# Performance work log

Hardware: AMD Instinct MI355X
Metric: run time of the kernel (lower is better)

Reference implementation:

```python
import jax, jax.numpy as jnp
import numpy as np

K = 8            # kernel volume = down_ratio^3 = 2^3
N_IN = 40000     # coarse (input) active voxels
N_OUT = 150000   # fine (output/skip) active voxels
C_IN = 128
C_EMB = 128
C_SKIP = 128
EPS = 1e-5


def setup_inputs() -> dict:
    key = jax.random.key(0)
    ks = jax.random.split(key, 8)
    x_feat = jax.random.normal(ks[0], (N_IN, C_IN), dtype=jnp.float32)
    skip_feat = jax.random.normal(ks[1], (N_OUT, C_SKIP), dtype=jnp.float32)
    pair_in = jax.random.randint(ks[2], (K, N_OUT), 0, N_IN, dtype=jnp.int32)
    pair_out = jax.random.randint(ks[3], (K, N_OUT), 0, N_OUT, dtype=jnp.int32)
    W_up = jax.random.normal(ks[4], (K, C_IN, C_EMB), dtype=jnp.float32) * 0.02
    W1 = jax.random.normal(ks[5], (C_SKIP + C_EMB, C_EMB), dtype=jnp.float32) * 0.05
    W2 = jax.random.normal(ks[6], (C_EMB, C_EMB), dtype=jnp.float32) * 0.05
    return {
        "x_feat": x_feat, "skip_feat": skip_feat,
        "pair_in": pair_in, "pair_out": pair_out,
        "W_up": W_up,
        "g0": jnp.ones((C_EMB,), jnp.float32), "b0": jnp.zeros((C_EMB,), jnp.float32),
        "W1": W1, "b1": jnp.zeros((C_EMB,), jnp.float32),
        "g1": jnp.ones((C_EMB,), jnp.float32), "be1": jnp.zeros((C_EMB,), jnp.float32),
        "W2": W2, "b2": jnp.zeros((C_EMB,), jnp.float32),
        "g2": jnp.ones((C_EMB,), jnp.float32), "be2": jnp.zeros((C_EMB,), jnp.float32),
    }


def _bn(x, gamma, beta):
    # BatchNorm1d over the point axis (training-mode batch stats, biased var)
    m = jnp.mean(x, axis=0)
    v = jnp.mean(jnp.square(x - m), axis=0)
    return (x - m) * jax.lax.rsqrt(v + EPS) * gamma + beta


def reference(x_feat, skip_feat, pair_in, pair_out, W_up,
              g0, b0, W1, b1, g1, be1, W2, b2, g2, be2):
    n_out = skip_feat.shape[0]
    # SparseInverseConv3d: gather coarse features, per-offset GEMM, scatter-add
    out = jnp.zeros((n_out, W_up.shape[2]), dtype=x_feat.dtype)
    for k in range(K):  # fixed small kernel volume, structurally distinct weights
        contrib = x_feat[pair_in[k]] @ W_up[k]          # [P, C_emb]
        out = out.at[pair_out[k]].add(contrib)
    up = jax.nn.relu(_bn(out, g0, b0))                  # [N_out, C_emb]

    # fuse: concat([up, skip]) -> Linear/BN/ReLU x2, residual with up
    h = jnp.concatenate([up, skip_feat], axis=1)        # [N_out, C_emb+C_skip]
    h = jax.nn.relu(_bn(h @ W1 + b1, g1, be1))
    h = jax.nn.relu(_bn(h @ W2 + b2, g2, be2))
    return h + up
```

## Files before the change

### kernel.cpp

```cpp
#include <hip/hip_runtime.h>

#define KVOL 8
#define NIN 40000
#define NOUT 150000
#define C 128
#define EPSV 1e-5f
#define NPAIR (KVOL * NOUT)
#define GM ((NOUT + 63) / 64)
#define GM2 ((NOUT + 127) / 128)
#define GUP (NIN / 64)
#define BROWS 128
#define NBUCK ((NOUT + BROWS - 1) / BROWS)
#define NSTR 8
#define SCAP 256
#define BCAP (NSTR * SCAP)
#define GBUCK ((NPAIR + 4095) / 4096)
#define GUPB (GBUCK + GUP)

typedef __attribute__((ext_vector_type(8))) __bf16 bf16x8;
typedef __attribute__((ext_vector_type(4))) float f32x4;
typedef __attribute__((ext_vector_type(8))) unsigned short us8;

__device__ __forceinline__ unsigned short fbf(float f) {
    unsigned u = __float_as_uint(f);
    u += 0x7fffu + ((u >> 16) & 1u);
    return (unsigned short)(u >> 16);
}
__device__ __forceinline__ float bff(unsigned short s) {
    return __uint_as_float(((unsigned)s) << 16);
}

__global__ __launch_bounds__(256) void k_prep_w(
    const float* __restrict__ Wup, const float* __restrict__ W1, const float* __restrict__ W2,
    unsigned short* __restrict__ WT)
{
    int i = blockIdx.x * 256 + threadIdx.x;
    if (i < 11 * 16384) {
        int b = i >> 14, r = i & 16383;
        int k = r >> 7, n = r & 127;
        const float* src = (b < 8) ? (Wup + (size_t)b * 16384)
                         : (b < 10) ? (W1 + (size_t)(b - 8) * 16384) : W2;
        WT[(size_t)b * 16384 + n * 128 + k] = fbf(src[k * 128 + n]);
    }
}

__global__ __launch_bounds__(256) void k_upb(
    const float* __restrict__ x, const unsigned short* __restrict__ WT,
    unsigned short* __restrict__ Y,
    const int* __restrict__ pout, const int* __restrict__ pin,
    int* __restrict__ bcnt, unsigned int* __restrict__ bbuf)
{
    __shared__ __align__(16) unsigned short Alds[64][136];
    __shared__ __align__(16) unsigned short Wlds[128][136];
    const int t = threadIdx.x;

    if (blockIdx.x < GBUCK) {
        int* cnt = (int*)&Alds[0][0];
        int* bas = cnt + NBUCK;
        int* run = bas + NBUCK;
        const int bid = blockIdx.x;
        const int str = bid & (NSTR - 1);
        const int i0 = bid * 4096;
        for (int b = t; b < NBUCK; b += 256) { cnt[b] = 0; run[b] = 0; }
        __syncthreads();
        for (int j = t; j < 4096; j += 256) {
            int i = i0 + j;
            if (i < NPAIR) atomicAdd(&cnt[pout[i] >> 7], 1);
        }
        __syncthreads();
        for (int b = t; b < NBUCK; b += 256) {
            int c = cnt[b];
            bas[b] = c ? atomicAdd(&bcnt[str * NBUCK + b], c) : 0;
        }
        __syncthreads();
        for (int j = t; j < 4096; j += 256) {
            int i = i0 + j;
            if (i < NPAIR) {
                int o = pout[i];
                int k = i / NOUT;
                unsigned e = (unsigned)(k * NIN + pin[i]);
                int b = o >> 7;
                int dst = bas[b] + atomicAdd(&run[b], 1);
                if (dst < SCAP)
                    bbuf[((size_t)str * NBUCK + b) * SCAP + dst] = ((unsigned)(o & 127) << 24) | e;
            }
        }
        return;
    }

    const int wave = t >> 6, lane = t & 63;
    const int l15 = lane & 15, lhi = lane >> 4;
    const int R = (blockIdx.x - GBUCK) * 64;
    const float4* A4 = (const float4*)x;
    #pragma unroll
    for (int j = 0; j < 8; ++j) {
        int idx = t + j * 256;
        int row = idx >> 5, c4 = idx & 31;
        int grow = R + row;
        float4 v = make_float4(0.f, 0.f, 0.f, 0.f);
        if (grow < NIN) v = A4[(size_t)grow * 32 + c4];
        ushort4 o;
        o.x = fbf(v.x); o.y = fbf(v.y); o.z = fbf(v.z); o.w = fbf(v.w);
        *(ushort4*)&Alds[row][c4 * 4] = o;
    }
    __syncthreads();
    bf16x8 af[4];
    #pragma unroll
    for (int kk = 0; kk < 4; ++kk)
        af[kk] = *(const bf16x8*)&Alds[wave * 16 + l15][kk * 32 + lhi * 8];
    for (int k = 0; k < KVOL; ++k) {
        __syncthreads();
        const us8* Wsrc = (const us8*)(WT + (size_t)k * C * C);
        #pragma unroll
        for (int j = 0; j < 8; ++j) {
            int slot = t + j * 256;
            int n = slot >> 4, koff = (slot & 15) * 8;
            *(us8*)&Wlds[n][koff] = Wsrc[slot];
        }
        __syncthreads();
        f32x4 acc[8];
        #pragma unroll
        for (int n = 0; n < 8; ++n) acc[n] = (f32x4){0.f, 0.f, 0.f, 0.f};
        #pragma unroll
        for (int n = 0; n < 8; ++n) {
            #pragma unroll
            for (int kk = 0; kk < 4; ++kk) {
                bf16x8 bfr = *(const bf16x8*)&Wlds[n * 16 + l15][kk * 32 + lhi * 8];
                acc[n] = __builtin_amdgcn_mfma_f32_16x16x32_bf16(af[kk], bfr, acc[n], 0, 0, 0);
            }
        }
        unsigned short* Yk = Y + (size_t)k * NIN * C;
        #pragma unroll
        for (int n = 0; n < 8; ++n) {
            const int col = n * 16 + l15;
            #pragma unroll
            for (int r = 0; r < 4; ++r) {
                int row = R + wave * 16 + lhi * 4 + r;
                if (row < NIN) Yk[(size_t)row * C + col] = fbf(acc[n][r]);
            }
        }
    }
}

template<int PHASES, bool BNIN, bool STATS>
__global__ __launch_bounds__(512) void k_mfma(
    const void* __restrict__ A0v, const void* __restrict__ A1v,
    const unsigned short* __restrict__ WT,
    const float* __restrict__ bias,
    unsigned short* __restrict__ outp, int M,
    const float* __restrict__ bn_stats, const float* __restrict__ bn_g, const float* __restrict__ bn_b,
    float* __restrict__ parts)
{
    __shared__ __align__(16) unsigned short Alds[128][136];
    __shared__ __align__(16) unsigned short Wlds[128][136];
    __shared__ float sscale[C], sshift[C];
    const int t = threadIdx.x;
    const int wave = t >> 6, lane = t & 63;
    const int l15 = lane & 15, lhi = lane >> 4;
    const int R = blockIdx.x * 128;

    if (BNIN) {
        if (t < C) {
            float m = bn_stats[t] * (1.0f / NOUT);
            float var = bn_stats[C + t] * (1.0f / NOUT) - m * m;
            float sc = bn_g[t] * rsqrtf(var + EPSV);
            sscale[t] = sc;
            sshift[t] = fmaf(-m, sc, bn_b[t]);
        }
        __syncthreads();
    }

    f32x4 acc[8];
    #pragma unroll
    for (int n = 0; n < 8; ++n) acc[n] = (f32x4){0.f, 0.f, 0.f, 0.f};

    {
        const us8* Wsrc = (const us8*)WT;
        #pragma unroll
        for (int j = 0; j < 4; ++j) {
            int slot = t + j * 512;
            *(us8*)&Wlds[slot >> 4][(slot & 15) * 8] = Wsrc[slot];
        }
        const us8* A8 = (const us8*)A0v;
        #pragma unroll
        for (int j = 0; j < 4; ++j) {
            int slot = t + j * 512;
            int row = slot >> 4, s15 = slot & 15, koff = s15 * 8;
            int grow = R + row;
            us8 v = (us8){0, 0, 0, 0, 0, 0, 0, 0};
            if (grow < M) v = A8[(size_t)grow * 16 + s15];
            if (BNIN) {
                us8 w;
                #pragma unroll
                for (int i = 0; i < 8; ++i) {
                    float f = fmaxf(fmaf(bff(v[i]), sscale[koff + i], sshift[koff + i]), 0.f);
                    w[i] = fbf(f);
                }
                v = w;
            }
            *(us8*)&Alds[row][koff] = v;
        }
    }
    __syncthreads();

    if constexpr (PHASES == 2) {
        us8 wreg[4];
        float4 areg[8];
        {
            const us8* Wsrc1 = (const us8*)(WT + C * C);
            #pragma unroll
            for (int j = 0; j < 4; ++j) wreg[j] = Wsrc1[t + j * 512];
            const float4* A41 = (const float4*)A1v;
            #pragma unroll
            for (int j = 0; j < 8; ++j) {
                int slot = t + j * 512;
                int row = slot >> 5, c4 = slot & 31;
                int grow = R + row;
                float4 v = make_float4(0.f, 0.f, 0.f, 0.f);
                if (grow < M) v = A41[(size_t)grow * 32 + c4];
                areg[j] = v;
            }
        }
        {
            bf16x8 af[4];
            #pragma unroll
            for (int kk = 0; kk < 4; ++kk)
                af[kk] = *(const bf16x8*)&Alds[wave * 16 + l15][kk * 32 + lhi * 8];
            #pragma unroll
            for (int n = 0; n < 8; ++n) {
                #pragma unroll
                for (int kk = 0; kk < 4; ++kk) {
                    bf16x8 bfr = *(const bf16x8*)&Wlds[n * 16 + l15][kk * 32 + lhi * 8];
                    acc[n] = __builtin_amdgcn_mfma_f32_16x16x32_bf16(af[kk], bfr, acc[n], 0, 0, 0);
                }
            }
        }
        __syncthreads();
        #pragma unroll
        for (int j = 0; j < 4; ++j) {
            int slot = t + j * 512;
            *(us8*)&Wlds[slot >> 4][(slot & 15) * 8] = wreg[j];
        }
        #pragma unroll
        for (int j = 0; j < 8; ++j) {
            int slot = t + j * 512;
            int row = slot >> 5, c4 = slot & 31;
            float4 v = areg[j];
            ushort4 o;
            o.x = fbf(v.x); o.y = fbf(v.y); o.z = fbf(v.z); o.w = fbf(v.w);
            *(ushort4*)&Alds[row][c4 * 4] = o;
        }
        __syncthreads();
    }
    {
        bf16x8 af[4];
        #pragma unroll
        for (int kk = 0; kk < 4; ++kk)
            af[kk] = *(const bf16x8*)&Alds[wave * 16 + l15][kk * 32 + lhi * 8];
        #pragma unroll
        for (int n = 0; n < 8; ++n) {
            #pragma unroll
            for (int kk = 0; kk < 4; ++kk) {
                bf16x8 bfr = *(const bf16x8*)&Wlds[n * 16 + l15][kk * 32 + lhi * 8];
                acc[n] = __builtin_amdgcn_mfma_f32_16x16x32_bf16(af[kk], bfr, acc[n], 0, 0, 0);
            }
        }
    }
    __syncthreads();

    float* sbS = (float*)&Alds[0][0];
    float* sbQ = sbS + 1024;
    #pragma unroll
    for (int n = 0; n < 8; ++n) {
        const int col = n * 16 + l15;
        float bv = bias[col];
        float s = 0.f, q = 0.f;
        #pragma unroll
        for (int r = 0; r < 4; ++r) {
            int row = R + wave * 16 + lhi * 4 + r;
            if (row < M) {
                float v = acc[n][r] + bv;
                outp[(size_t)row * C + col] = fbf(v);
                if (STATS) { s += v; q = fmaf(v, v, q); }
            }
        }
        if (STATS) {
            s += __shfl_xor(s, 16); s += __shfl_xor(s, 32);
            q += __shfl_xor(q, 16); q += __shfl_xor(q, 32);
            if (lane < 16) {
                sbS[wave * 128 + col] = s;
                sbQ[wave * 128 + col] = q;
            }
        }
    }
    if (STATS) {
        __syncthreads();
        if (t < 128) {
            float S = 0.f;
            #pragma unroll
            for (int w = 0; w < 8; ++w) S += sbS[w * 128 + t];
            parts[(size_t)blockIdx.x * 256 + t] = S;
        } else if (t < 256) {
            int cc = t - 128;
            float Q = 0.f;
            #pragma unroll
            for (int w = 0; w < 8; ++w) Q += sbQ[w * 128 + cc];
            parts[(size_t)blockIdx.x * 256 + t] = Q;
        }
    }
}

__global__ __launch_bounds__(256) void k_reduce(const float* __restrict__ parts, int nb,
                                                float* __restrict__ stats)
{
    const int t = threadIdx.x;
    float s0 = 0.f, s1 = 0.f, s2 = 0.f, s3 = 0.f;
    for (int b = blockIdx.x * 4; b < nb; b += gridDim.x * 4) {
        if (b < nb)     s0 += parts[(size_t)b * 256 + t];
        if (b + 1 < nb) s1 += parts[(size_t)(b + 1) * 256 + t];
        if (b + 2 < nb) s2 += parts[(size_t)(b + 2) * 256 + t];
        if (b + 3 < nb) s3 += parts[(size_t)(b + 3) * 256 + t];
    }
    atomicAdd(&stats[t], (s0 + s1) + (s2 + s3));
}

__global__ __launch_bounds__(256) void k_sortgather(
    const int* __restrict__ bcnt, const unsigned int* __restrict__ bbuf,
    const us8* __restrict__ Y8, us8* __restrict__ up8, float* __restrict__ parts)
{
    __shared__ unsigned int pr[BCAP];
    __shared__ unsigned int srt[BCAP];
    __shared__ int cnt[BROWS], sd[BROWS], ofs2[BROWS];
    const int t = threadIdx.x;
    const int b = blockIdx.x;
    int segbase = 0;
    #pragma unroll
    for (int s = 0; s < NSTR; ++s) {
        int ns = min(bcnt[s * NBUCK + b], SCAP);
        const unsigned int* g = bbuf + ((size_t)s * NBUCK + b) * SCAP;
        for (int j = t; j < ns; j += 256) pr[segbase + j] = g[j];
        segbase += ns;
    }
    const int n = segbase;
    if (t < BROWS) cnt[t] = 0;
    __syncthreads();
    for (int j = t; j < n; j += 256) atomicAdd(&cnt[pr[j] >> 24], 1);
    __syncthreads();
    if (t < BROWS) sd[t] = cnt[t];
    __syncthreads();
    for (int off = 1; off < BROWS; off <<= 1) {
        int a = (t < BROWS) ? sd[t] : 0;
        int bb = (t < BROWS && t >= off) ? sd[t - off] : 0;
        __syncthreads();
        if (t < BROWS) sd[t] = a + bb;
        __syncthreads();
    }
    if (t < BROWS) ofs2[t] = sd[t] - cnt[t];
    __syncthreads();
    for (int j = t; j < n; j += 256) {
        unsigned p = pr[j];
        int pos = atomicAdd(&ofs2[p >> 24], 1);
        srt[pos] = p & 0xFFFFFFu;
    }
    __syncthreads();
    const int wave = t >> 6, lane = t & 63;
    const int rl = t >> 4, c8 = t & 15;
    float s8[8], q8[8];
    #pragma unroll
    for (int i = 0; i < 8; ++i) { s8[i] = 0.f; q8[i] = 0.f; }
    #pragma unroll
    for (int it = 0; it < 8; ++it) {
        int r = it * 16 + rl;
        int o = b * BROWS + r;
        if (o < NOUT) {
            int j1 = sd[r], j0 = j1 - cnt[r];
            float a[8];
            #pragma unroll
            for (int i = 0; i < 8; ++i) a[i] = 0.f;
            int j = j0;
            for (; j + 1 < j1; j += 2) {
                unsigned e0 = srt[j], e1 = srt[j + 1];
                us8 u0 = Y8[(size_t)e0 * 16 + c8];
                us8 u1 = Y8[(size_t)e1 * 16 + c8];
                #pragma unroll
                for (int i = 0; i < 8; ++i) a[i] += bff(u0[i]) + bff(u1[i]);
            }
            if (j < j1) {
                unsigned e0 = srt[j];
                us8 u0 = Y8[(size_t)e0 * 16 + c8];
                #pragma unroll
                for (int i = 0; i < 8; ++i) a[i] += bff(u0[i]);
            }
            us8 o8;
            #pragma unroll
            for (int i = 0; i < 8; ++i) {
                o8[i] = fbf(a[i]);
                s8[i] += a[i];
                q8[i] = fmaf(a[i], a[i], q8[i]);
            }
            up8[(size_t)o * 16 + c8] = o8;
        }
    }
    #pragma unroll
    for (int i = 0; i < 8; ++i) {
        s8[i] += __shfl_xor(s8[i], 16); s8[i] += __shfl_xor(s8[i], 32);
        q8[i] += __shfl_xor(q8[i], 16); q8[i] += __shfl_xor(q8[i], 32);
    }
    float* sS = (float*)pr;
    float* sQ = sS + 512;
    if (lane < 16) {
        #pragma unroll
        for (int i = 0; i < 8; ++i) {
            sS[(wave * 16 + c8) * 8 + i] = s8[i];
            sQ[(wave * 16 + c8) * 8 + i] = q8[i];
        }
    }
    __syncthreads();
    if (t < 128) {
        const int cc = t >> 3, ii = t & 7;
        float S = 0.f, Q = 0.f;
        #pragma unroll
        for (int w = 0; w < 4; ++w) {
            S += sS[(w * 16 + cc) * 8 + ii];
            Q += sQ[(w * 16 + cc) * 8 + ii];
        }
        parts[(size_t)b * 256 + t] = S;
        parts[(size_t)b * 256 + 128 + t] = Q;
    }
}

__global__ __launch_bounds__(256) void k_final(
    const us8* __restrict__ h2, const us8* __restrict__ upr, float* __restrict__ out,
    const float* __restrict__ stats2, const float* __restrict__ g2, const float* __restrict__ be2,
    const float* __restrict__ stats0, const float* __restrict__ g0, const float* __restrict__ b0)
{
    __shared__ float sc2[C], sh2[C], sc0[C], sh0[C];
    const int t = threadIdx.x;
    if (t < C) {
        float m2 = stats2[t] * (1.0f / NOUT);
        float v2 = stats2[C + t] * (1.0f / NOUT) - m2 * m2;
        float c2 = g2[t] * rsqrtf(v2 + EPSV);
        sc2[t] = c2; sh2[t] = fmaf(-m2, c2, be2[t]);
        float m0 = stats0[t] * (1.0f / NOUT);
        float v0 = stats0[C + t] * (1.0f / NOUT) - m0 * m0;
        float c0 = g0[t] * rsqrtf(v0 + EPSV);
        sc0[t] = c0; sh0[t] = fmaf(-m0, c0, b0[t]);
    }
    __syncthreads();
    const int idx0 = blockIdx.x * 256 + t;
    const int c8 = idx0 & 15;
    float l2s[8], l2h[8], l0s[8], l0h[8];
    #pragma unroll
    for (int i = 0; i < 8; ++i) {
        l2s[i] = sc2[c8 * 8 + i]; l2h[i] = sh2[c8 * 8 + i];
        l0s[i] = sc0[c8 * 8 + i]; l0h[i] = sh0[c8 * 8 + i];
    }
    const int total = NOUT * 16;
    for (int idx = idx0; idx < total; idx += gridDim.x * 256) {
        us8 h = h2[idx];
        us8 u = upr[idx];
        float o[8];
        #pragma unroll
        for (int i = 0; i < 8; ++i) {
            o[i] = fmaxf(fmaf(bff(h[i]), l2s[i], l2h[i]), 0.f)
                 + fmaxf(fmaf(bff(u[i]), l0s[i], l0h[i]), 0.f);
        }
        float4* dst = (float4*)&out[(size_t)idx * 8];
        dst[0] = make_float4(o[0], o[1], o[2], o[3]);
        dst[1] = make_float4(o[4], o[5], o[6], o[7]);
    }
}

extern "C" void kernel_launch(void* const* d_in, const int* in_sizes, int n_in,
                              void* d_out, int out_size, void* d_ws, size_t ws_size,
                              hipStream_t stream)
{
    const float* x    = (const float*)d_in[0];
    const float* skip = (const float*)d_in[1];
    const int*   pin  = (const int*)d_in[2];
    const int*   pout = (const int*)d_in[3];
    const float* Wup  = (const float*)d_in[4];
    const float* g0   = (const float*)d_in[5];
    const float* b0   = (const float*)d_in[6];
    const float* W1   = (const float*)d_in[7];
    const float* b1   = (const float*)d_in[8];
    const float* g1   = (const float*)d_in[9];
    const float* be1  = (const float*)d_in[10];
    const float* W2   = (const float*)d_in[11];
    const float* b2   = (const float*)d_in[12];
    const float* g2   = (const float*)d_in[13];
    const float* be2  = (const float*)d_in[14];
    float* outp = (float*)d_out;

    char* base = (char*)d_ws;
    unsigned short* Y      = (unsigned short*)base;
    unsigned short* h1     = (unsigned short*)base;
    unsigned short* h2     = (unsigned short*)(base + 40960000);
    unsigned short* up_raw = (unsigned short*)(base + 81920000);
    char* p = base + 81920000 + 38400000;
    unsigned short* WT = (unsigned short*)p; p += (size_t)11 * 16384 * 2;
    unsigned int* bbuf = (unsigned int*)p;  p += (size_t)NSTR * NBUCK * SCAP * 4;
    int* bcnt      = (int*)p; p += (size_t)NSTR * NBUCK * 4;
    float* parts0  = (float*)p; p += (size_t)NBUCK * 256 * 4;
    float* parts1  = (float*)p; p += (size_t)GM * 256 * 4;
    float* parts2  = (float*)p; p += (size_t)GM * 256 * 4;
    float* stats   = (float*)p; p += 3 * 256 * 4;

    hipMemsetAsync(bcnt, 0, (size_t)NSTR * NBUCK * 4, stream);
    hipMemsetAsync(stats, 0, 3 * 256 * 4, stream);

    k_prep_w<<<(11 * 16384 + 255) / 256, 256, 0, stream>>>(Wup, W1, W2, WT);

    k_upb<<<GUPB, 256, 0, stream>>>(x, WT, Y, pout, pin, bcnt, bbuf);

    k_sortgather<<<NBUCK, 256, 0, stream>>>(bcnt, bbuf, (const us8*)Y, (us8*)up_raw, parts0);
    k_reduce<<<16, 256, 0, stream>>>(parts0, NBUCK, stats);

    k_mfma<2, true, true><<<GM2, 512, 0, stream>>>(
        up_raw, skip, WT + (size_t)8 * 16384, b1, h1, NOUT, stats, g0, b0, parts1);
    k_reduce<<<16, 256, 0, stream>>>(parts1, GM2, stats + 256);

    k_mfma<1, true, true><<<GM2, 512, 0, stream>>>(
        h1, nullptr, WT + (size_t)10 * 16384, b2, h2, NOUT, stats + 256, g1, be1, parts2);
    k_reduce<<<16, 256, 0, stream>>>(parts2, GM2, stats + 512);

    k_final<<<1024, 256, 0, stream>>>((const us8*)h2, (const us8*)up_raw, outp,
        stats + 512, g2, be2, stats, g0, b0);
}
```

Before: 301.5 us.

## Split bucketing from up-GEMM, halve bucket size, stage GEMM outputs through LDS

Splits the fused bucket/up-projection kernel into two separate launches and halves the output-row bucket size (and its per-stream capacity), which doubles the number of sort-gather blocks and halves the rows each one handles. Both the up-projection and the fused MLP GEMM kernels now write bf16 results into LDS first, then store them as coalesced 16-byte vector rows instead of scattered 2-byte stores. This trades extra barriers and LDS traffic for wider global writes, and adds one more kernel launch. The smaller bucket capacity raises the risk of overflow (dropped pairs) if a bucket receives too many entries.

```diff
diff --git a/kernel.cpp b/kernel.cpp
--- a/kernel.cpp
+++ b/kernel.cpp
@@ -9,13 +9,12 @@
 #define GM ((NOUT + 63) / 64)
 #define GM2 ((NOUT + 127) / 128)
 #define GUP (NIN / 64)
-#define BROWS 128
+#define BROWS 64
 #define NBUCK ((NOUT + BROWS - 1) / BROWS)
 #define NSTR 8
-#define SCAP 256
+#define SCAP 128
 #define BCAP (NSTR * SCAP)
 #define GBUCK ((NPAIR + 4095) / 4096)
-#define GUPB (GBUCK + GUP)
 
 typedef __attribute__((ext_vector_type(8))) __bf16 bf16x8;
 typedef __attribute__((ext_vector_type(4))) float f32x4;
@@ -44,53 +43,52 @@
     }
 }
 
-__global__ __launch_bounds__(256) void k_upb(
-    const float* __restrict__ x, const unsigned short* __restrict__ WT,
-    unsigned short* __restrict__ Y,
+__global__ __launch_bounds__(256) void k_bucket2(
     const int* __restrict__ pout, const int* __restrict__ pin,
     int* __restrict__ bcnt, unsigned int* __restrict__ bbuf)
+{
+    __shared__ int cnt[NBUCK];
+    __shared__ int bas[NBUCK];
+    __shared__ int run[NBUCK];
+    const int t = threadIdx.x;
+    const int str = blockIdx.x & (NSTR - 1);
+    const int i0 = blockIdx.x * 4096;
+    for (int b = t; b < NBUCK; b += 256) { cnt[b] = 0; run[b] = 0; }
+    __syncthreads();
+    for (int j = t; j < 4096; j += 256) {
+        int i = i0 + j;
+        if (i < NPAIR) atomicAdd(&cnt[pout[i] >> 6], 1);
+    }
+    __syncthreads();
+    for (int b = t; b < NBUCK; b += 256) {
+        int c = cnt[b];
+        bas[b] = c ? atomicAdd(&bcnt[str * NBUCK + b], c) : 0;
+    }
+    __syncthreads();
+    for (int j = t; j < 4096; j += 256) {
+        int i = i0 + j;
+        if (i < NPAIR) {
+            int o = pout[i];
+            int k = i / NOUT;
+            unsigned e = (unsigned)(k * NIN + pin[i]);
+            int b = o >> 6;
+            int dst = bas[b] + atomicAdd(&run[b], 1);
+            if (dst < SCAP)
+                bbuf[((size_t)str * NBUCK + b) * SCAP + dst] = ((unsigned)(o & 63) << 24) | e;
+        }
+    }
+}
+
+__global__ __launch_bounds__(256) void k_up(
+    const float* __restrict__ x, const unsigned short* __restrict__ WT,
+    unsigned short* __restrict__ Y)
 {
     __shared__ __align__(16) unsigned short Alds[64][136];
     __shared__ __align__(16) unsigned short Wlds[128][136];
     const int t = threadIdx.x;
-
-    if (blockIdx.x < GBUCK) {
-        int* cnt = (int*)&Alds[0][0];
-        int* bas = cnt + NBUCK;
-        int* run = bas + NBUCK;
-        const int bid = blockIdx.x;
-        const int str = bid & (NSTR - 1);
-        const int i0 = bid * 4096;
-        for (int b = t; b < NBUCK; b += 256) { cnt[b] = 0; run[b] = 0; }
-        __syncthreads();
-        for (int j = t; j < 4096; j += 256) {
-            int i = i0 + j;
-            if (i < NPAIR) atomicAdd(&cnt[pout[i] >> 7], 1);
-        }
-        __syncthreads();
-        for (int b = t; b < NBUCK; b += 256) {
-            int c = cnt[b];
-            bas[b] = c ? atomicAdd(&bcnt[str * NBUCK + b], c) : 0;
-        }
-        __syncthreads();
-        for (int j = t; j < 4096; j += 256) {
-            int i = i0 + j;
-            if (i < NPAIR) {
-                int o = pout[i];
-                int k = i / NOUT;
-                unsigned e = (unsigned)(k * NIN + pin[i]);
-                int b = o >> 7;
-                int dst = bas[b] + atomicAdd(&run[b], 1);
-                if (dst < SCAP)
-                    bbuf[((size_t)str * NBUCK + b) * SCAP + dst] = ((unsigned)(o & 127) << 24) | e;
-            }
-        }
-        return;
-    }
-
     const int wave = t >> 6, lane = t & 63;
     const int l15 = lane & 15, lhi = lane >> 4;
-    const int R = (blockIdx.x - GBUCK) * 64;
+    const int R = blockIdx.x * 64;
     const float4* A4 = (const float4*)x;
     #pragma unroll
     for (int j = 0; j < 8; ++j) {
@@ -108,6 +106,7 @@
     #pragma unroll
     for (int kk = 0; kk < 4; ++kk)
         af[kk] = *(const bf16x8*)&Alds[wave * 16 + l15][kk * 32 + lhi * 8];
+    unsigned short* scr = (unsigned short*)&Wlds[0][0];
     for (int k = 0; k < KVOL; ++k) {
         __syncthreads();
         const us8* Wsrc = (const us8*)(WT + (size_t)k * C * C);
@@ -129,15 +128,21 @@
                 acc[n] = __builtin_amdgcn_mfma_f32_16x16x32_bf16(af[kk], bfr, acc[n], 0, 0, 0);
             }
         }
-        unsigned short* Yk = Y + (size_t)k * NIN * C;
+        __syncthreads();
         #pragma unroll
         for (int n = 0; n < 8; ++n) {
             const int col = n * 16 + l15;
             #pragma unroll
-            for (int r = 0; r < 4; ++r) {
-                int row = R + wave * 16 + lhi * 4 + r;
-                if (row < NIN) Yk[(size_t)row * C + col] = fbf(acc[n][r]);
-            }
+            for (int r = 0; r < 4; ++r)
+                scr[(wave * 16 + lhi * 4 + r) * 136 + col] = fbf(acc[n][r]);
+        }
+        __syncthreads();
+        us8* Yk8 = (us8*)(Y + (size_t)k * NIN * C);
+        #pragma unroll
+        for (int j = 0; j < 4; ++j) {
+            int slot = t + j * 256;
+            int lrow = slot >> 4, c8 = slot & 15;
+            Yk8[(size_t)(R + lrow) * 16 + c8] = *(const us8*)&scr[lrow * 136 + c8 * 8];
         }
     }
 }
@@ -268,6 +273,7 @@
     }
     __syncthreads();
 
+    unsigned short* scr = (unsigned short*)&Wlds[0][0];
     float* sbS = (float*)&Alds[0][0];
     float* sbQ = sbS + 1024;
     #pragma unroll
@@ -277,12 +283,10 @@
         float s = 0.f, q = 0.f;
         #pragma unroll
         for (int r = 0; r < 4; ++r) {
-            int row = R + wave * 16 + lhi * 4 + r;
-            if (row < M) {
-                float v = acc[n][r] + bv;
-                outp[(size_t)row * C + col] = fbf(v);
-                if (STATS) { s += v; q = fmaf(v, v, q); }
-            }
+            int lrow = wave * 16 + lhi * 4 + r;
+            float v = acc[n][r] + bv;
+            scr[lrow * 136 + col] = fbf(v);
+            if (STATS && (R + lrow) < M) { s += v; q = fmaf(v, v, q); }
         }
         if (STATS) {
             s += __shfl_xor(s, 16); s += __shfl_xor(s, 32);
@@ -293,8 +297,16 @@
             }
         }
     }
+    __syncthreads();
+    us8* out8 = (us8*)outp;
+    #pragma unroll
+    for (int j = 0; j < 4; ++j) {
+        int slot = t + j * 512;
+        int lrow = slot >> 4, c8 = slot & 15;
+        int grow = R + lrow;
+        if (grow < M) out8[(size_t)grow * 16 + c8] = *(const us8*)&scr[lrow * 136 + c8 * 8];
+    }
     if (STATS) {
-        __syncthreads();
         if (t < 128) {
             float S = 0.f;
             #pragma unroll
@@ -369,7 +381,7 @@
     #pragma unroll
     for (int i = 0; i < 8; ++i) { s8[i] = 0.f; q8[i] = 0.f; }
     #pragma unroll
-    for (int it = 0; it < 8; ++it) {
+    for (int it = 0; it < 4; ++it) {
         int r = it * 16 + rl;
         int o = b * BROWS + r;
         if (o < NOUT) {
@@ -511,7 +523,9 @@
 
     k_prep_w<<<(11 * 16384 + 255) / 256, 256, 0, stream>>>(Wup, W1, W2, WT);
 
-    k_upb<<<GUPB, 256, 0, stream>>>(x, WT, Y, pout, pin, bcnt, bbuf);
+    k_bucket2<<<GBUCK, 256, 0, stream>>>(pout, pin, bcnt, bbuf);
+
+    k_up<<<GUP, 256, 0, stream>>>(x, WT, Y);
 
     k_sortgather<<<NBUCK, 256, 0, stream>>>(bcnt, bbuf, (const us8*)Y, (us8*)up_raw, parts0);
     k_reduce<<<16, 256, 0, stream>>>(parts0, NBUCK, stats);
```

New measurement: 330.2 us. 9.5% more time.

## Swap MFMA operands for row-contiguous vector stores and split bucket kernel

Applied to the files above, without the earlier changes.

Swaps the A and B operands of the bf16 MFMA so each lane holds four consecutive output columns of one row. This lets the GEMM epilogues write 8-byte vector stores instead of scattered 2-byte stores, and changes the BN statistics reduction to a 16-lane shuffle tree. The fused bucket/up-projection launch is also split into two separate kernels, which gives each its own LDS footprint but removes their overlap within a single launch. The bounds checks in the up-projection load are dropped because NIN is a multiple of 64.

```diff
diff --git a/kernel.cpp b/kernel.cpp
--- a/kernel.cpp
+++ b/kernel.cpp
@@ -15,7 +15,6 @@
 #define SCAP 256
 #define BCAP (NSTR * SCAP)
 #define GBUCK ((NPAIR + 4095) / 4096)
-#define GUPB (GBUCK + GUP)
 
 typedef __attribute__((ext_vector_type(8))) __bf16 bf16x8;
 typedef __attribute__((ext_vector_type(4))) float f32x4;
@@ -44,61 +43,58 @@
     }
 }
 
-__global__ __launch_bounds__(256) void k_upb(
-    const float* __restrict__ x, const unsigned short* __restrict__ WT,
-    unsigned short* __restrict__ Y,
+__global__ __launch_bounds__(256) void k_bucket2(
     const int* __restrict__ pout, const int* __restrict__ pin,
     int* __restrict__ bcnt, unsigned int* __restrict__ bbuf)
+{
+    __shared__ int cnt[NBUCK];
+    __shared__ int bas[NBUCK];
+    __shared__ int run[NBUCK];
+    const int t = threadIdx.x;
+    const int str = blockIdx.x & (NSTR - 1);
+    const int i0 = blockIdx.x * 4096;
+    for (int b = t; b < NBUCK; b += 256) { cnt[b] = 0; run[b] = 0; }
+    __syncthreads();
+    for (int j = t; j < 4096; j += 256) {
+        int i = i0 + j;
+        if (i < NPAIR) atomicAdd(&cnt[pout[i] >> 7], 1);
+    }
+    __syncthreads();
+    for (int b = t; b < NBUCK; b += 256) {
+        int c = cnt[b];
+        bas[b] = c ? atomicAdd(&bcnt[str * NBUCK + b], c) : 0;
+    }
+    __syncthreads();
+    for (int j = t; j < 4096; j += 256) {
+        int i = i0 + j;
+        if (i < NPAIR) {
+            int o = pout[i];
+            int k = i / NOUT;
+            unsigned e = (unsigned)(k * NIN + pin[i]);
+            int b = o >> 7;
+            int dst = bas[b] + atomicAdd(&run[b], 1);
+            if (dst < SCAP)
+                bbuf[((size_t)str * NBUCK + b) * SCAP + dst] = ((unsigned)(o & 127) << 24) | e;
+        }
+    }
+}
+
+__global__ __launch_bounds__(256) void k_up(
+    const float* __restrict__ x, const unsigned short* __restrict__ WT,
+    unsigned short* __restrict__ Y)
 {
     __shared__ __align__(16) unsigned short Alds[64][136];
     __shared__ __align__(16) unsigned short Wlds[128][136];
     const int t = threadIdx.x;
-
-    if (blockIdx.x < GBUCK) {
-        int* cnt = (int*)&Alds[0][0];
-        int* bas = cnt + NBUCK;
-        int* run = bas + NBUCK;
-        const int bid = blockIdx.x;
-        const int str = bid & (NSTR - 1);
-        const int i0 = bid * 4096;
-        for (int b = t; b < NBUCK; b += 256) { cnt[b] = 0; run[b] = 0; }
-        __syncthreads();
-        for (int j = t; j < 4096; j += 256) {
-            int i = i0 + j;
-            if (i < NPAIR) atomicAdd(&cnt[pout[i] >> 7], 1);
-        }
-        __syncthreads();
-        for (int b = t; b < NBUCK; b += 256) {
-            int c = cnt[b];
-            bas[b] = c ? atomicAdd(&bcnt[str * NBUCK + b], c) : 0;
-        }
-        __syncthreads();
-        for (int j = t; j < 4096; j += 256) {
-            int i = i0 + j;
-            if (i < NPAIR) {
-                int o = pout[i];
-                int k = i / NOUT;
-                unsigned e = (unsigned)(k * NIN + pin[i]);
-                int b = o >> 7;
-                int dst = bas[b] + atomicAdd(&run[b], 1);
-                if (dst < SCAP)
-                    bbuf[((size_t)str * NBUCK + b) * SCAP + dst] = ((unsigned)(o & 127) << 24) | e;
-            }
-        }
-        return;
-    }
-
     const int wave = t >> 6, lane = t & 63;
     const int l15 = lane & 15, lhi = lane >> 4;
-    const int R = (blockIdx.x - GBUCK) * 64;
+    const int R = blockIdx.x * 64;
     const float4* A4 = (const float4*)x;
     #pragma unroll
     for (int j = 0; j < 8; ++j) {
         int idx = t + j * 256;
         int row = idx >> 5, c4 = idx & 31;
-        int grow = R + row;
-        float4 v = make_float4(0.f, 0.f, 0.f, 0.f);
-        if (grow < NIN) v = A4[(size_t)grow * 32 + c4];
+        float4 v = A4[(size_t)(R + row) * 32 + c4];
         ushort4 o;
         o.x = fbf(v.x); o.y = fbf(v.y); o.z = fbf(v.z); o.w = fbf(v.w);
         *(ushort4*)&Alds[row][c4 * 4] = o;
@@ -108,6 +104,7 @@
     #pragma unroll
     for (int kk = 0; kk < 4; ++kk)
         af[kk] = *(const bf16x8*)&Alds[wave * 16 + l15][kk * 32 + lhi * 8];
+    const int orow = R + wave * 16 + l15;
     for (int k = 0; k < KVOL; ++k) {
         __syncthreads();
         const us8* Wsrc = (const us8*)(WT + (size_t)k * C * C);
@@ -126,18 +123,15 @@
             #pragma unroll
             for (int kk = 0; kk < 4; ++kk) {
                 bf16x8 bfr = *(const bf16x8*)&Wlds[n * 16 + l15][kk * 32 + lhi * 8];
-                acc[n] = __builtin_amdgcn_mfma_f32_16x16x32_bf16(af[kk], bfr, acc[n], 0, 0, 0);
+                acc[n] = __builtin_amdgcn_mfma_f32_16x16x32_bf16(bfr, af[kk], acc[n], 0, 0, 0);
             }
         }
         unsigned short* Yk = Y + (size_t)k * NIN * C;
         #pragma unroll
         for (int n = 0; n < 8; ++n) {
-            const int col = n * 16 + l15;
-            #pragma unroll
-            for (int r = 0; r < 4; ++r) {
-                int row = R + wave * 16 + lhi * 4 + r;
-                if (row < NIN) Yk[(size_t)row * C + col] = fbf(acc[n][r]);
-            }
+            ushort4 o = make_ushort4(fbf(acc[n][0]), fbf(acc[n][1]),
+                                     fbf(acc[n][2]), fbf(acc[n][3]));
+            *(ushort4*)&Yk[(size_t)orow * C + n * 16 + lhi * 4] = o;
         }
     }
 }
@@ -231,7 +225,7 @@
                 #pragma unroll
                 for (int kk = 0; kk < 4; ++kk) {
                     bf16x8 bfr = *(const bf16x8*)&Wlds[n * 16 + l15][kk * 32 + lhi * 8];
-                    acc[n] = __builtin_amdgcn_mfma_f32_16x16x32_bf16(af[kk], bfr, acc[n], 0, 0, 0);
+                    acc[n] = __builtin_amdgcn_mfma_f32_16x16x32_bf16(bfr, af[kk], acc[n], 0, 0, 0);
                 }
             }
         }
@@ -262,7 +256,7 @@
             #pragma unroll
             for (int kk = 0; kk < 4; ++kk) {
                 bf16x8 bfr = *(const bf16x8*)&Wlds[n * 16 + l15][kk * 32 + lhi * 8];
-                acc[n] = __builtin_amdgcn_mfma_f32_16x16x32_bf16(af[kk], bfr, acc[n], 0, 0, 0);
+                acc[n] = __builtin_amdgcn_mfma_f32_16x16x32_bf16(bfr, af[kk], acc[n], 0, 0, 0);
             }
         }
     }
@@ -270,26 +264,34 @@
 
     float* sbS = (float*)&Alds[0][0];
     float* sbQ = sbS + 1024;
+    const int orow = R + wave * 16 + l15;
+    const bool ok = orow < M;
     #pragma unroll
     for (int n = 0; n < 8; ++n) {
-        const int col = n * 16 + l15;
-        float bv = bias[col];
-        float s = 0.f, q = 0.f;
-        #pragma unroll
-        for (int r = 0; r < 4; ++r) {
-            int row = R + wave * 16 + lhi * 4 + r;
-            if (row < M) {
-                float v = acc[n][r] + bv;
-                outp[(size_t)row * C + col] = fbf(v);
-                if (STATS) { s += v; q = fmaf(v, v, q); }
-            }
+        const float4 bv4 = *(const float4*)&bias[n * 16 + lhi * 4];
+        float v0 = acc[n][0] + bv4.x;
+        float v1 = acc[n][1] + bv4.y;
+        float v2 = acc[n][2] + bv4.z;
+        float v3 = acc[n][3] + bv4.w;
+        if (ok) {
+            ushort4 o = make_ushort4(fbf(v0), fbf(v1), fbf(v2), fbf(v3));
+            *(ushort4*)&outp[(size_t)orow * C + n * 16 + lhi * 4] = o;
         }
         if (STATS) {
-            s += __shfl_xor(s, 16); s += __shfl_xor(s, 32);
-            q += __shfl_xor(q, 16); q += __shfl_xor(q, 32);
-            if (lane < 16) {
-                sbS[wave * 128 + col] = s;
-                sbQ[wave * 128 + col] = q;
+            float s0 = ok ? v0 : 0.f, s1 = ok ? v1 : 0.f;
+            float s2 = ok ? v2 : 0.f, s3 = ok ? v3 : 0.f;
+            float q0 = s0 * s0, q1 = s1 * s1, q2 = s2 * s2, q3 = s3 * s3;
+            #pragma unroll
+            for (int m = 1; m < 16; m <<= 1) {
+                s0 += __shfl_xor(s0, m); s1 += __shfl_xor(s1, m);
+                s2 += __shfl_xor(s2, m); s3 += __shfl_xor(s3, m);
+                q0 += __shfl_xor(q0, m); q1 += __shfl_xor(q1, m);
+                q2 += __shfl_xor(q2, m); q3 += __shfl_xor(q3, m);
+            }
+            if (l15 == 0) {
+                int cb = wave * 128 + n * 16 + lhi * 4;
+                sbS[cb + 0] = s0; sbS[cb + 1] = s1; sbS[cb + 2] = s2; sbS[cb + 3] = s3;
+                sbQ[cb + 0] = q0; sbQ[cb + 1] = q1; sbQ[cb + 2] = q2; sbQ[cb + 3] = q3;
             }
         }
     }
@@ -511,7 +513,9 @@
 
     k_prep_w<<<(11 * 16384 + 255) / 256, 256, 0, stream>>>(Wup, W1, W2, WT);
 
-    k_upb<<<GUPB, 256, 0, stream>>>(x, WT, Y, pout, pin, bcnt, bbuf);
+    k_bucket2<<<GBUCK, 256, 0, stream>>>(pout, pin, bcnt, bbuf);
+
+    k_up<<<GUP, 256, 0, stream>>>(x, WT, Y);
 
     k_sortgather<<<NBUCK, 256, 0, stream>>>(bcnt, bbuf, (const us8*)Y, (us8*)up_raw, parts0);
     k_reduce<<<16, 256, 0, stream>>>(parts0, NBUCK, stats);
```

Measured after the change: 334.4 us. +10.9%, slower.
